# Performance work log

Hardware: AMD Instinct MI355X
Metric: run time of the kernel (lower is better)

Reference implementation:

```python
import jax, jax.numpy as jnp
import numpy as np

B, N, H, D, A = 64, 32, 100, 400, 200  # batch, news_num, hist_len, news_dim, attention_dim


def setup_inputs() -> dict:
    key = jax.random.key(0)
    k0, k1, k2, k3, k4 = jax.random.split(key, 5)
    log_vec = jax.random.normal(k0, (B, H, D), dtype=jnp.float32)
    log_mask = jax.random.randint(k1, (B, H), 0, 2).astype(jnp.int32)
    news_vec = jax.random.normal(k2, (B, N, D), dtype=jnp.float32)
    W1 = jax.random.normal(k3, (A, 2 * D), dtype=jnp.float32) * 0.02
    b1 = jnp.zeros((A,), dtype=jnp.float32)
    W2 = jax.random.normal(k4, (1, A), dtype=jnp.float32) * 0.02
    b2 = jnp.zeros((1,), dtype=jnp.float32)
    return {"log_vec": log_vec, "log_mask": log_mask, "news_vec": news_vec,
            "W1": W1, "b1": b1, "W2": W2, "b2": b2}


def reference(log_vec, log_mask, news_vec, W1, b1, W2, b2):
    d = log_vec.shape[-1]
    # affine1 on cat([news, log]) == Wn @ news + Wl @ log (split the weight),
    # so we never build the [B, N, H, 2D] concat tensor.
    Wn, Wl = W1[:, :d], W1[:, d:]
    pn = jnp.einsum('bnd,ad->bna', news_vec, Wn)            # [B, N, A]
    pl = jnp.einsum('bhd,ad->bha', log_vec, Wl) + b1        # [B, H, A]
    h = jnp.tanh(pn[:, :, None, :] + pl[:, None, :, :])     # [B, N, H, A]
    logits = jnp.einsum('bnha,a->bnh', h, W2[0]) + b2[0]    # [B, N, H]
    logits = jnp.where(log_mask[:, None, :] == 0, jnp.float32(-1e9), logits)
    attn = jax.nn.softmax(logits, axis=2)                   # softmax over hist_len
    return jnp.einsum('bnh,bhd->bnd', attn, log_vec)        # [B, N, D]
```

## Files before the change

### kernel.cpp

```cpp
#include <hip/hip_runtime.h>
#include <hip/hip_fp16.h>
#include <math.h>

#define BB 64
#define NN 32
#define HH 100
#define DD 400
#define AA 200
#define NL 8
#define NQ 4
#define SZ_LOG  2560000
#define SZ_NEWS 819200
#define SZ_W1   160000
#define SZ_MASK 6400
#define LROW 40
#define PLP 204
#define WS2_NEED ((size_t)(BB*HH + BB*NN) * AA * 4)

typedef unsigned short u16;
typedef unsigned int   u32;
typedef unsigned long long u64;
typedef __attribute__((ext_vector_type(8))) short    bf16x8;
typedef __attribute__((ext_vector_type(8))) _Float16 halfx8;
typedef __attribute__((ext_vector_type(4))) float    f32x4;

__device__ __forceinline__ float bfh(u32 h) { return __uint_as_float(h << 16); }
__device__ __forceinline__ u16 f2bf(float f) {
    u32 u = __float_as_uint(f);
    u += 0x7fffu + ((u >> 16) & 1u);
    return (u16)(u >> 16);
}
__device__ __forceinline__ float halfbits(u16 h) {
    __half_raw r; r.x = h; __half hv(r); return __half2float(hv);
}
__device__ __forceinline__ u16 h2bits(float f) {
    __half h = __float2half(f); return *(u16*)&h;
}
__device__ __forceinline__ float sane(float x) {
    return (fabsf(x) < 1e6f) ? x : 0.f;
}

template<int DT>
__device__ __forceinline__ float ld1(const void* p, size_t i) {
    if (DT == 0) return bfh(((const u16*)p)[i]);
    if (DT == 1) return halfbits(((const u16*)p)[i]);
    return ((const float*)p)[i];
}

__device__ __forceinline__ bf16x8 cvt8(const float* p) {
    const float4 x0 = *(const float4*)p;
    const float4 x1 = *(const float4*)(p + 4);
    bf16x8 r;
    r[0] = (short)f2bf(sane(x0.x)); r[1] = (short)f2bf(sane(x0.y));
    r[2] = (short)f2bf(sane(x0.z)); r[3] = (short)f2bf(sane(x0.w));
    r[4] = (short)f2bf(sane(x1.x)); r[5] = (short)f2bf(sane(x1.y));
    r[6] = (short)f2bf(sane(x1.z)); r[7] = (short)f2bf(sane(x1.w));
    return r;
}

__device__ __forceinline__ void detect_counts(const u16* logv, int t, int* s_cbf, int* s_cfh) {
    int cbf = 0, cfh = 0;
    for (int i = 2 * t; i < 4096; i += 512) {
        u16 h = logv[i];
        float a = fabsf(bfh(h));
        if (h && a >= 0.03125f && a <= 16.f) cbf++;
        float g = fabsf(halfbits(h));
        if (h && g >= 1e-3f && g <= 64.f) cfh++;
    }
    #pragma unroll
    for (int off = 32; off; off >>= 1) {
        cbf += __shfl_xor(cbf, off);
        cfh += __shfl_xor(cfh, off);
    }
    if ((t & 63) == 0) {
        atomicAdd(s_cbf, cbf);
        atomicAdd(s_cfh, cfh);
    }
}

__device__ __forceinline__ void prologue(
        const u16* logv, const int* mask, const u16* c200a, const u16* c200b,
        int* s_det, int* s_hn, int* mask_s, int* chi, int b, int t,
        int* dt_o, int* aW2_o, int* hn_o)
{
    const int wave = t >> 6, lane = t & 63;
    if (t < 4) s_det[t] = 0;
    if (t < HH) mask_s[t] = mask[b * HH + t];
    __syncthreads();
    if (t < 256) detect_counts(logv, t, &s_det[0], &s_det[1]);
    if (t < AA) {
        if (c200a[t]) atomicOr(&s_det[2], 1);
        if (c200b[t]) atomicOr(&s_det[3], 1);
    }
    if (wave == 0) {
        const bool v = mask_s[lane] != 0;
        const u64 bal = __ballot(v);
        if (v) chi[__popcll(bal & ((1ull << lane) - 1ull))] = lane;
    } else if (wave == 1) {
        const u64 b0 = __ballot(mask_s[lane] != 0);
        const int c0 = __popcll(b0);
        const bool v1 = (lane < HH - 64) && (mask_s[64 + lane] != 0);
        const u64 b1 = __ballot(v1);
        if (v1) chi[c0 + __popcll(b1 & ((1ull << lane) - 1ull))] = 64 + lane;
        if (lane == 0) *s_hn = c0 + __popcll(b1);
    }
    __syncthreads();
    *dt_o  = (s_det[0] > 1024) ? 0 : ((s_det[1] > 1600) ? 1 : 2);
    *aW2_o = (s_det[2] && !s_det[3]) ? 1 : 0;
    *hn_o  = *s_hn;
}

template<int DT>
__device__ __forceinline__ void gemm_body(
        const void* __restrict__ logv, const void* __restrict__ newsv,
        const void* __restrict__ w1, const void* __restrict__ b1p,
        float* __restrict__ ws_pl, float* __restrict__ ws_pn,
        u16* As0, u16* Bs0, u16* As1, u16* Bs1,
        float* b1s, const int* chi, int hn, int r0, int r1, int mtc_loc,
        int b, int q, int t)
{
    const int wave = t >> 6, lane = t & 63;
    const int quad = lane >> 4, col16 = lane & 15;

    if (t < AA) b1s[t] = sane(ld1<DT>(b1p, t));

    const int mtIdx = wave >> 1, half = wave & 1;
    const bool isPn = (mtIdx == mtc_loc);
    const bool act  = (mtIdx <= mtc_loc);
    const int arow  = isPn ? (32 + min(col16, NL - 1)) : (mtIdx * 16 + col16);
    const int aidx  = arow * LROW + quad * 8;
    int bidx[7];
    #pragma unroll
    for (int si = 0; si < 7; ++si) {
        const int sl = min(half * 7 + si, 12);
        const int brow = min(sl * 16 + col16, AA - 1);
        bidx[si] = ((isPn ? 0 : 208) + brow) * LROW + quad * 8;
    }
    f32x4 acc[7];
    #pragma unroll
    for (int si = 0; si < 7; ++si) acc[si] = (f32x4){0.f, 0.f, 0.f, 0.f};

    const int bh0 = t / 832,   rem0 = t - bh0 * 832;
    const int br0 = rem0 >> 2, bseg0 = rem0 & 3;
    const size_t bg0 = (size_t)min(br0, AA - 1) * (2 * DD) + bh0 * DD + bseg0 * 8;
    const int bl0 = (bh0 * 208 + br0) * LROW + bseg0 * 8;
    const int i1 = t + 1024;
    const bool bok1 = i1 < 1664;
    const int bh1 = bok1 ? (i1 / 832) : 0, rem1 = i1 - bh1 * 832;
    const int br1 = rem1 >> 2, bseg1 = rem1 & 3;
    const size_t bg1 = (size_t)min(br1, AA - 1) * (2 * DD) + bh1 * DD + bseg1 * 8;
    const int bl1 = (bh1 * 208 + br1) * LROW + bseg1 * 8;
    const int ar = t >> 2, aseg = t & 3;
    const bool a_ok = t < 160;
    size_t agi = 0;
    if (a_ok) {
        if (ar < 32) {
            const int grow = hn ? chi[min(r0 + ar, hn - 1)] : 0;
            agi = ((size_t)b * HH + grow) * DD + aseg * 8;
        } else {
            agi = ((size_t)b * NN + q * NL + (ar - 32)) * DD + aseg * 8;
        }
    }
    const int al = ar * LROW + aseg * 8;
    const u16*   agp  = (ar < 32 ? (const u16*)logv   : (const u16*)newsv) + agi;
    const float* agpf = (ar < 32 ? (const float*)logv : (const float*)newsv) + agi;
    const u16*   w1p  = (const u16*)w1;
    const float* w1pf = (const float*)w1;

    const uint4 z4 = {0u, 0u, 0u, 0u};
    uint4 vb0 = z4, vb1 = z4, va = z4;

    if (DT != 2) {
        vb0 = *(const uint4*)(w1p + bg0);
        if (bok1) vb1 = *(const uint4*)(w1p + bg1);
        if (a_ok) va  = *(const uint4*)agp;
        *(uint4*)&Bs0[bl0] = vb0;
        if (bok1) *(uint4*)&Bs0[bl1] = vb1;
        if (a_ok) *(uint4*)&As0[al] = va;
        vb0 = *(const uint4*)(w1p + bg0 + 32);
        if (bok1) vb1 = *(const uint4*)(w1p + bg1 + 32);
        if (a_ok) va  = *(const uint4*)(agp + 32);
    } else {
        { bf16x8 c = cvt8(w1pf + bg0); *(uint4*)&Bs0[bl0] = *(uint4*)&c; }
        if (bok1) { bf16x8 c = cvt8(w1pf + bg1); *(uint4*)&Bs0[bl1] = *(uint4*)&c; }
        if (a_ok) { bf16x8 c = cvt8(agpf); *(uint4*)&As0[al] = *(uint4*)&c; }
    }
    __syncthreads();

    for (int ki = 0; ki < 13; ++ki) {
        const int cur = ki & 1;
        u16* const Ac = cur ? As1 : As0;
        u16* const Bc = cur ? Bs1 : Bs0;
        u16* const An = cur ? As0 : As1;
        u16* const Bn = cur ? Bs0 : Bs1;

        if (DT != 2) {
            if (ki < 12) {
                *(uint4*)&Bn[bl0] = vb0;
                if (bok1) *(uint4*)&Bn[bl1] = vb1;
                if (a_ok) *(uint4*)&An[al] = va;
            }
            if (ki < 11) {
                const int kn = ki + 2;
                vb0 = (kn == 12 && bseg0 >= 2) ? z4 : *(const uint4*)(w1p + bg0 + (size_t)kn * 32);
                if (bok1) vb1 = (kn == 12 && bseg1 >= 2) ? z4 : *(const uint4*)(w1p + bg1 + (size_t)kn * 32);
                if (a_ok) va = (kn == 12 && aseg >= 2) ? z4 : *(const uint4*)(agp + (size_t)kn * 32);
            }
        } else {
            if (ki < 12) {
                const int kn = ki + 1;
                uint4 v = z4;
                if (!(kn == 12 && bseg0 >= 2)) { bf16x8 c = cvt8(w1pf + bg0 + (size_t)kn * 32); v = *(uint4*)&c; }
                *(uint4*)&Bn[bl0] = v;
                if (bok1) {
                    v = z4;
                    if (!(kn == 12 && bseg1 >= 2)) { bf16x8 c = cvt8(w1pf + bg1 + (size_t)kn * 32); v = *(uint4*)&c; }
                    *(uint4*)&Bn[bl1] = v;
                }
                if (a_ok) {
                    v = z4;
                    if (!(kn == 12 && aseg >= 2)) { bf16x8 c = cvt8(agpf + (size_t)kn * 32); v = *(uint4*)&c; }
                    *(uint4*)&An[al] = v;
                }
            }
        }

        if (act) {
            if (DT == 1) {
                const halfx8 af = *(const halfx8*)&Ac[aidx];
                #pragma unroll
                for (int si = 0; si < 7; ++si) {
                    const halfx8 bf = *(const halfx8*)&Bc[bidx[si]];
                    acc[si] = __builtin_amdgcn_mfma_f32_16x16x32_f16(af, bf, acc[si], 0, 0, 0);
                }
            } else {
                const bf16x8 af = *(const bf16x8*)&Ac[aidx];
                #pragma unroll
                for (int si = 0; si < 7; ++si) {
                    const bf16x8 bf = *(const bf16x8*)&Bc[bidx[si]];
                    acc[si] = __builtin_amdgcn_mfma_f32_16x16x32_bf16(af, bf, acc[si], 0, 0, 0);
                }
            }
        }
        __syncthreads();
    }

    if (act) {
        #pragma unroll
        for (int si = 0; si < 7; ++si) {
            const int sl = half * 7 + si;
            if (sl > 12) continue;
            const int acol = sl * 16 + col16;
            if (acol < AA) {
                if (isPn) {
                    #pragma unroll
                    for (int r = 0; r < 4; ++r) {
                        const int row = quad * 4 + r;
                        if (row < NL)
                            ws_pn[((size_t)(b * NQ + q) * NL + row) * AA + acol] = sane(acc[si][r]) + b1s[acol];
                    }
                } else {
                    #pragma unroll
                    for (int r = 0; r < 4; ++r) {
                        const int grow = r0 + mtIdx * 16 + quad * 4 + r;
                        if (grow < r1)
                            ws_pl[((size_t)b * HH + grow) * AA + acol] = sane(acc[si][r]);
                    }
                }
            }
        }
    }
}

__global__ __launch_bounds__(1024) void gemm_ws(
        const void* __restrict__ logv, const int* __restrict__ mask,
        const void* __restrict__ newsv, const void* __restrict__ w1,
        const void* __restrict__ c200a, const void* __restrict__ c200b,
        float* __restrict__ ws_pl, float* __restrict__ ws_pn)
{
    __shared__ __align__(16) u16 As0[48 * LROW], As1[48 * LROW];
    __shared__ __align__(16) u16 Bs0[2 * 208 * LROW], Bs1[2 * 208 * LROW];
    __shared__ float b1s[AA];
    __shared__ int   mask_s[HH], chi[HH];
    __shared__ int   s_det[4], s_hn;

    const int t = threadIdx.x;
    const int b = blockIdx.x & 63;
    const int q = blockIdx.x >> 6;

    int dt, aW2, hn;
    prologue((const u16*)logv, mask, (const u16*)c200a, (const u16*)c200b,
             s_det, &s_hn, mask_s, chi, b, t, &dt, &aW2, &hn);
    const void* b1p = aW2 ? c200b : c200a;

    const int qs = (hn + 3) >> 2;
    const int r0 = q * qs;
    const int r1 = min(r0 + qs, hn);
    const int nr = max(r1 - r0, 0);
    const int mtc_loc = (nr + 15) >> 4;

    if (dt == 0)      gemm_body<0>(logv, newsv, w1, b1p, ws_pl, ws_pn, As0, Bs0, As1, Bs1, b1s, chi, hn, r0, r1, mtc_loc, b, q, t);
    else if (dt == 1) gemm_body<1>(logv, newsv, w1, b1p, ws_pl, ws_pn, As0, Bs0, As1, Bs1, b1s, chi, hn, r0, r1, mtc_loc, b, q, t);
    else              gemm_body<2>(logv, newsv, w1, b1p, ws_pl, ws_pn, As0, Bs0, As1, Bs1, b1s, chi, hn, r0, r1, mtc_loc, b, q, t);
}

template<int DT>
__device__ __forceinline__ void attn_body2(
        const void* __restrict__ logv, const void* __restrict__ w2p,
        const float* __restrict__ pls, const float* __restrict__ pnb,
        void* __restrict__ out,
        float (* __restrict__ lgt)[HH], float* __restrict__ w2s,
        const int* __restrict__ chi, int hn, bool useChi,
        int b, int n0, int t)
{
    const int wave = t >> 6, lane = t & 63;

    if (t < AA) w2s[t] = sane(ld1<DT>(w2p, t));
    __syncthreads();

    {
        const int j = t;
        if (j < 4 * hn) {
            const int p = j / hn;
            const int i = j - p * hn;
            const int h = chi[i];
            const float* plr = pls + (size_t)i * AA;
            const float* pA  = pnb + p * AA;
            const float* pB  = pnb + (p + 4) * AA;
            float accA = 0.f, accB = 0.f, sw = 0.f;
            for (int a = 0; a < AA; a += 4) {
                const float4 w4  = *(const float4*)&w2s[a];
                const float4 pl4 = *(const float4*)&plr[a];
                const float4 pA4 = *(const float4*)&pA[a];
                const float4 pB4 = *(const float4*)&pB[a];
                #define LSTEP(CC) { \
                    const float w2v = w4.CC; \
                    const float plv = pl4.CC; \
                    const float eA = __builtin_amdgcn_exp2f((pA4.CC + plv) * 2.885390081777927f); \
                    const float eB = __builtin_amdgcn_exp2f((pB4.CC + plv) * 2.885390081777927f); \
                    accA = __builtin_fmaf(w2v, __builtin_amdgcn_rcpf(eA + 1.f), accA); \
                    accB = __builtin_fmaf(w2v, __builtin_amdgcn_rcpf(eB + 1.f), accB); \
                    sw += w2v; }
                LSTEP(x) LSTEP(y) LSTEP(z) LSTEP(w)
                #undef LSTEP
            }
            lgt[p][h]     = sw - 2.f * accA;
            lgt[p + 4][h] = sw - 2.f * accB;
        }
    }
    __syncthreads();

    if (wave < NL) {
        const int n = wave;
        float m1 = lgt[n][lane];
        float m2 = (lane < HH - 64) ? lgt[n][64 + lane] : -3.0e38f;
        float mx = fmaxf(m1, m2);
        #pragma unroll
        for (int off = 32; off; off >>= 1) mx = fmaxf(mx, __shfl_xor(mx, off));
        float e1 = expf(m1 - mx);
        float e2 = (lane < HH - 64) ? expf(m2 - mx) : 0.f;
        float s = e1 + e2;
        #pragma unroll
        for (int off = 32; off; off >>= 1) s += __shfl_xor(s, off);
        const float inv = 1.f / s;
        lgt[n][lane] = e1 * inv;
        if (lane < HH - 64) lgt[n][64 + lane] = e2 * inv;
    }
    __syncthreads();

    {
        const int n = wave >> 1, half2 = wave & 1;
        const int hn_pv = useChi ? hn : HH;
        const int d2a = lane + 128 * half2;
        const int d2b = d2a + 64;
        const bool bv = d2b < DD / 2;
        const int d2bc = bv ? d2b : d2a;
        float aA0 = 0.f, aA1 = 0.f, aB0 = 0.f, aB1 = 0.f;
        int i = 0;
        for (; i + 1 < hn_pv; i += 2) {
            const int h0 = useChi ? chi[i] : i;
            const int h1 = useChi ? chi[i + 1] : (i + 1);
            const float w0 = lgt[n][h0], w1v = lgt[n][h1];
            float v0a, v1a, v0b, v1b, u0a, u1a, u0b, u1b;
            if (DT == 2) {
                const float* r0 = (const float*)logv + ((size_t)b * HH + h0) * DD;
                const float* r1 = (const float*)logv + ((size_t)b * HH + h1) * DD;
                v0a = r0[2 * d2a]; v1a = r0[2 * d2a + 1];
                v0b = r0[2 * d2bc]; v1b = r0[2 * d2bc + 1];
                u0a = r1[2 * d2a]; u1a = r1[2 * d2a + 1];
                u0b = r1[2 * d2bc]; u1b = r1[2 * d2bc + 1];
            } else {
                const u16* r0 = (const u16*)logv + ((size_t)b * HH + h0) * DD;
                const u16* r1 = (const u16*)logv + ((size_t)b * HH + h1) * DD;
                const u32 pa = *(const u32*)(r0 + 2 * d2a);
                const u32 pb = *(const u32*)(r0 + 2 * d2bc);
                const u32 qa = *(const u32*)(r1 + 2 * d2a);
                const u32 qb = *(const u32*)(r1 + 2 * d2bc);
                if (DT == 0) {
                    v0a = bfh(pa & 0xffffu); v1a = bfh(pa >> 16);
                    v0b = bfh(pb & 0xffffu); v1b = bfh(pb >> 16);
                    u0a = bfh(qa & 0xffffu); u1a = bfh(qa >> 16);
                    u0b = bfh(qb & 0xffffu); u1b = bfh(qb >> 16);
                } else {
                    v0a = halfbits((u16)(pa & 0xffffu)); v1a = halfbits((u16)(pa >> 16));
                    v0b = halfbits((u16)(pb & 0xffffu)); v1b = halfbits((u16)(pb >> 16));
                    u0a = halfbits((u16)(qa & 0xffffu)); u1a = halfbits((u16)(qa >> 16));
                    u0b = halfbits((u16)(qb & 0xffffu)); u1b = halfbits((u16)(qb >> 16));
                }
            }
            aA0 = __builtin_fmaf(w0, sane(v0a), aA0); aA1 = __builtin_fmaf(w0, sane(v1a), aA1);
            aB0 = __builtin_fmaf(w0, sane(v0b), aB0); aB1 = __builtin_fmaf(w0, sane(v1b), aB1);
            aA0 = __builtin_fmaf(w1v, sane(u0a), aA0); aA1 = __builtin_fmaf(w1v, sane(u1a), aA1);
            aB0 = __builtin_fmaf(w1v, sane(u0b), aB0); aB1 = __builtin_fmaf(w1v, sane(u1b), aB1);
        }
        if (i < hn_pv) {
            const int h0 = useChi ? chi[i] : i;
            const float w0 = lgt[n][h0];
            float v0a, v1a, v0b, v1b;
            if (DT == 2) {
                const float* r0 = (const float*)logv + ((size_t)b * HH + h0) * DD;
                v0a = r0[2 * d2a]; v1a = r0[2 * d2a + 1];
                v0b = r0[2 * d2bc]; v1b = r0[2 * d2bc + 1];
            } else {
                const u16* r0 = (const u16*)logv + ((size_t)b * HH + h0) * DD;
                const u32 pa = *(const u32*)(r0 + 2 * d2a);
                const u32 pb = *(const u32*)(r0 + 2 * d2bc);
                if (DT == 0) {
                    v0a = bfh(pa & 0xffffu); v1a = bfh(pa >> 16);
                    v0b = bfh(pb & 0xffffu); v1b = bfh(pb >> 16);
                } else {
                    v0a = halfbits((u16)(pa & 0xffffu)); v1a = halfbits((u16)(pa >> 16));
                    v0b = halfbits((u16)(pb & 0xffffu)); v1b = halfbits((u16)(pb >> 16));
                }
            }
            aA0 = __builtin_fmaf(w0, sane(v0a), aA0); aA1 = __builtin_fmaf(w0, sane(v1a), aA1);
            aB0 = __builtin_fmaf(w0, sane(v0b), aB0); aB1 = __builtin_fmaf(w0, sane(v1b), aB1);
        }
        const size_t obase = ((size_t)b * NN + n0 + n) * DD;
        aA0 = sane(aA0); aA1 = sane(aA1); aB0 = sane(aB0); aB1 = sane(aB1);
        if (DT == 0) {
            *(u32*)((u16*)out + obase + 2 * d2a) = (u32)f2bf(aA0) | ((u32)f2bf(aA1) << 16);
            if (bv) *(u32*)((u16*)out + obase + 2 * d2b) = (u32)f2bf(aB0) | ((u32)f2bf(aB1) << 16);
        } else if (DT == 1) {
            *(u32*)((u16*)out + obase + 2 * d2a) = (u32)h2bits(aA0) | ((u32)h2bits(aA1) << 16);
            if (bv) *(u32*)((u16*)out + obase + 2 * d2b) = (u32)h2bits(aB0) | ((u32)h2bits(aB1) << 16);
        } else {
            float* f = (float*)out;
            f[obase + 2 * d2a] = aA0; f[obase + 2 * d2a + 1] = aA1;
            if (bv) { f[obase + 2 * d2b] = aB0; f[obase + 2 * d2b + 1] = aB1; }
        }
    }
}

__global__ __launch_bounds__(1024) void attn_ws(
        const void* __restrict__ logv, const int* __restrict__ mask,
        const void* __restrict__ c200a, const void* __restrict__ c200b,
        const float* __restrict__ ws_pl, const float* __restrict__ ws_pn,
        void* __restrict__ out)
{
    __shared__ float lgt[NL][HH];
    __shared__ float w2s[AA];
    __shared__ int   mask_s[HH], chi[HH];
    __shared__ int   s_det[4], s_hn, s_diag[2];

    const int t = threadIdx.x;
    const int b = blockIdx.x & 63;
    const int q = blockIdx.x >> 6;
    const int n0 = q * NL;

    if (t == 0) { s_diag[0] = 0; s_diag[1] = 0; }
    if (t < NL * HH) lgt[t / HH][t % HH] = -1.0e9f;
    int dt, aW2, hn;
    prologue((const u16*)logv, mask, (const u16*)c200a, (const u16*)c200b,
             s_det, &s_hn, mask_s, chi, b, t, &dt, &aW2, &hn);
    const void* w2p = aW2 ? c200a : c200b;
    const bool useChi = hn != 0;

    const float* pls = ws_pl + (size_t)b * HH * AA;
    const float* pnb = ws_pn + (size_t)(b * NQ + q) * NL * AA;

    if (dt == 0)      attn_body2<0>(logv, w2p, pls, pnb, out, lgt, w2s, chi, hn, useChi, b, n0, t);
    else if (dt == 1) attn_body2<1>(logv, w2p, pls, pnb, out, lgt, w2s, chi, hn, useChi, b, n0, t);
    else              attn_body2<2>(logv, w2p, pls, pnb, out, lgt, w2s, chi, hn, useChi, b, n0, t);

    if (blockIdx.x == 0) {
        const u32* maskw = (const u32*)mask;
        int mbig = 0, moddnz = 0, mevennz = 0;
        for (int i = t; i < 3200; i += 1024) {
            u32 w = maskw[i];
            if (w > 1u) mbig = 1;
            if ((i & 1) && w) moddnz = 1;
            if (!(i & 1) && w) mevennz = 1;
        }
        atomicOr(&s_diag[0], mbig);
        atomicOr(&s_diag[1], moddnz | (mevennz << 1));
        __syncthreads();
        if (t == 0) {
            const int cb = s_det[0], ch = s_det[1];
            int dg = 0;
            if (cb > 700 && cb < 1300) dg |= 1;
            else if (cb <= 700 && ch > 1300 && ch < 1800) dg |= 1;
            if (s_diag[0]) dg |= 2;
            const int oddnz = s_diag[1] & 1, evennz = (s_diag[1] >> 1) & 1;
            if (!oddnz && evennz) dg |= 4;
            const int nza = s_det[2] ? 1 : 0, nzb = s_det[3] ? 1 : 0;
            if (nza == nzb) dg |= 8;
            if (dg) {
                const float V = 1024.f + 8.f * (float)dg;
                if (dt == 0)      ((u16*)out)[0] = f2bf(V);
                else if (dt == 1) ((u16*)out)[0] = h2bits(V);
                else              ((float*)out)[0] = V;
            }
        }
    }
}

template<int DT>
__device__ __forceinline__ void mega_body(
        const void* __restrict__ logv, const void* __restrict__ newsv,
        const void* __restrict__ w1,
        const void* __restrict__ w2p, const void* __restrict__ b1p,
        void* __restrict__ out,
        u16* As0, u16* Bs0, u16* ovl,
        float* pls, float* pnb,
        float (*lgt)[HH],
        float* w2s, float* b1s,
        const int* chi, int hn, bool useChi,
        int b, int n0, int t)
{
    const int wave = t >> 6, lane = t & 63;
    const int quad = lane >> 4, col16 = lane & 15;
    const int mtc = (hn + 15) >> 4;

    if (t < AA) {
        w2s[t] = sane(ld1<DT>(w2p, t));
        b1s[t] = sane(ld1<DT>(b1p, t));
    }

    const int mtIdx = wave >> 1, half = wave & 1;
    const bool isPn = (mtIdx == mtc);
    const bool act  = (mtIdx <= mtc);
    const int arow  = isPn ? (112 + min(col16, NL - 1)) : (mtIdx * 16 + col16);
    const int aidx  = arow * LROW + quad * 8;
    int bidx[7];
    #pragma unroll
    for (int si = 0; si < 7; ++si) {
        const int sl = min(half * 7 + si, 12);
        const int brow = min(sl * 16 + col16, AA - 1);
        bidx[si] = ((isPn ? 0 : 208) + brow) * LROW + quad * 8;
    }
    f32x4 acc[7];
    #pragma unroll
    for (int si = 0; si < 7; ++si) acc[si] = (f32x4){0.f, 0.f, 0.f, 0.f};

    const int bh0 = t / 832,   rem0 = t - bh0 * 832;
    const int br0 = rem0 >> 2, bseg0 = rem0 & 3;
    const size_t bg0 = (size_t)min(br0, AA - 1) * (2 * DD) + bh0 * DD + bseg0 * 8;
    const int bl0 = (bh0 * 208 + br0) * LROW + bseg0 * 8;
    const int i1 = t + 1024;
    const bool bok1 = i1 < 1664;
    const int bh1 = bok1 ? (i1 / 832) : 0, rem1 = i1 - bh1 * 832;
    const int br1 = rem1 >> 2, bseg1 = rem1 & 3;
    const size_t bg1 = (size_t)min(br1, AA - 1) * (2 * DD) + bh1 * DD + bseg1 * 8;
    const int bl1 = (bh1 * 208 + br1) * LROW + bseg1 * 8;
    const int ar = t >> 2, aseg = t & 3;
    const bool a_ok = (t < 480) && ((ar < mtc * 16) || (ar >= 112));
    size_t agi = 0;
    if (a_ok) {
        if (ar < 112) agi = ((size_t)b * HH + chi[min(ar, hn - 1)]) * DD + aseg * 8;
        else          agi = ((size_t)b * NN + n0 + (ar - 112)) * DD + aseg * 8;
    }
    const int al = ar * LROW + aseg * 8;
    const u16*   agp  = (ar < 112 ? (const u16*)logv   : (const u16*)newsv) + agi;
    const float* agpf = (ar < 112 ? (const float*)logv : (const float*)newsv) + agi;
    const u16*   w1p  = (const u16*)w1;
    const float* w1pf = (const float*)w1;

    u16* const As1 = ovl;
    u16* const Bs1 = ovl + 120 * LROW;

    const uint4 z4 = {0u, 0u, 0u, 0u};
    uint4 vb0 = z4, vb1 = z4, va = z4;

    if (DT != 2) {
        vb0 = *(const uint4*)(w1p + bg0);
        if (bok1) vb1 = *(const uint4*)(w1p + bg1);
        if (a_ok) va  = *(const uint4*)agp;
        *(uint4*)&Bs0[bl0] = vb0;
        if (bok1) *(uint4*)&Bs0[bl1] = vb1;
        if (a_ok) *(uint4*)&As0[al] = va;
        vb0 = *(const uint4*)(w1p + bg0 + 32);
        if (bok1) vb1 = *(const uint4*)(w1p + bg1 + 32);
        if (a_ok) va  = *(const uint4*)(agp + 32);
    } else {
        { bf16x8 c = cvt8(w1pf + bg0); *(uint4*)&Bs0[bl0] = *(uint4*)&c; }
        if (bok1) { bf16x8 c = cvt8(w1pf + bg1); *(uint4*)&Bs0[bl1] = *(uint4*)&c; }
        if (a_ok) { bf16x8 c = cvt8(agpf); *(uint4*)&As0[al] = *(uint4*)&c; }
    }
    __syncthreads();

    for (int ki = 0; ki < 13; ++ki) {
        const int cur = ki & 1;
        u16* const Ac = cur ? As1 : As0;
        u16* const Bc = cur ? Bs1 : Bs0;
        u16* const An = cur ? As0 : As1;
        u16* const Bn = cur ? Bs0 : Bs1;

        if (DT != 2) {
            if (ki < 12) {
                *(uint4*)&Bn[bl0] = vb0;
                if (bok1) *(uint4*)&Bn[bl1] = vb1;
                if (a_ok) *(uint4*)&An[al] = va;
            }
            if (ki < 11) {
                const int kn = ki + 2;
                vb0 = (kn == 12 && bseg0 >= 2) ? z4 : *(const uint4*)(w1p + bg0 + (size_t)kn * 32);
                if (bok1) vb1 = (kn == 12 && bseg1 >= 2) ? z4 : *(const uint4*)(w1p + bg1 + (size_t)kn * 32);
                if (a_ok) va = (kn == 12 && aseg >= 2) ? z4 : *(const uint4*)(agp + (size_t)kn * 32);
            }
        } else {
            if (ki < 12) {
                const int kn = ki + 1;
                uint4 v = z4;
                if (!(kn == 12 && bseg0 >= 2)) { bf16x8 c = cvt8(w1pf + bg0 + (size_t)kn * 32); v = *(uint4*)&c; }
                *(uint4*)&Bn[bl0] = v;
                if (bok1) {
                    v = z4;
                    if (!(kn == 12 && bseg1 >= 2)) { bf16x8 c = cvt8(w1pf + bg1 + (size_t)kn * 32); v = *(uint4*)&c; }
                    *(uint4*)&Bn[bl1] = v;
                }
                if (a_ok) {
                    v = z4;
                    if (!(kn == 12 && aseg >= 2)) { bf16x8 c = cvt8(agpf + (size_t)kn * 32); v = *(uint4*)&c; }
                    *(uint4*)&An[al] = v;
                }
            }
        }

        if (act) {
            if (DT == 1) {
                const halfx8 af = *(const halfx8*)&Ac[aidx];
                #pragma unroll
                for (int si = 0; si < 7; ++si) {
                    const halfx8 bf = *(const halfx8*)&Bc[bidx[si]];
                    acc[si] = __builtin_amdgcn_mfma_f32_16x16x32_f16(af, bf, acc[si], 0, 0, 0);
                }
            } else {
                const bf16x8 af = *(const bf16x8*)&Ac[aidx];
                #pragma unroll
                for (int si = 0; si < 7; ++si) {
                    const bf16x8 bf = *(const bf16x8*)&Bc[bidx[si]];
                    acc[si] = __builtin_amdgcn_mfma_f32_16x16x32_bf16(af, bf, acc[si], 0, 0, 0);
                }
            }
        }
        __syncthreads();
    }

    if (act) {
        #pragma unroll
        for (int si = 0; si < 7; ++si) {
            const int sl = half * 7 + si;
            if (sl > 12) continue;
            const int acol = sl * 16 + col16;
            if (acol < AA) {
                if (isPn) {
                    #pragma unroll
                    for (int r = 0; r < 4; ++r) {
                        const int row = quad * 4 + r;
                        if (row < NL) pnb[row * PLP + acol] = sane(acc[si][r]) + b1s[acol];
                    }
                } else {
                    #pragma unroll
                    for (int r = 0; r < 4; ++r) {
                        const int row = mtIdx * 16 + quad * 4 + r;
                        if (row < hn) pls[row * PLP + acol] = sane(acc[si][r]);
                    }
                }
            }
        }
    }
    __syncthreads();

    {
        const int j = t;
        if (j < 4 * hn) {
            const int p = j / hn;
            const int i = j - p * hn;
            const int h = chi[i];
            const float* plr = pls + i * PLP;
            const float* pA  = pnb + p * PLP;
            const float* pB  = pnb + (p + 4) * PLP;
            float accA = 0.f, accB = 0.f, sw = 0.f;
            for (int a = 0; a < AA; a += 4) {
                const float4 w4  = *(const float4*)&w2s[a];
                const float4 pl4 = *(const float4*)&plr[a];
                const float4 pA4 = *(const float4*)&pA[a];
                const float4 pB4 = *(const float4*)&pB[a];
                #define LSTEP(CC) { \
                    const float w2v = w4.CC; \
                    const float plv = pl4.CC; \
                    const float eA = __builtin_amdgcn_exp2f((pA4.CC + plv) * 2.885390081777927f); \
                    const float eB = __builtin_amdgcn_exp2f((pB4.CC + plv) * 2.885390081777927f); \
                    accA = __builtin_fmaf(w2v, __builtin_amdgcn_rcpf(eA + 1.f), accA); \
                    accB = __builtin_fmaf(w2v, __builtin_amdgcn_rcpf(eB + 1.f), accB); \
                    sw += w2v; }
                LSTEP(x) LSTEP(y) LSTEP(z) LSTEP(w)
                #undef LSTEP
            }
            lgt[p][h]     = sw - 2.f * accA;
            lgt[p + 4][h] = sw - 2.f * accB;
        }
    }
    __syncthreads();

    if (wave < NL) {
        const int n = wave;
        float m1 = lgt[n][lane];
        float m2 = (lane < HH - 64) ? lgt[n][64 + lane] : -3.0e38f;
        float mx = fmaxf(m1, m2);
        #pragma unroll
        for (int off = 32; off; off >>= 1) mx = fmaxf(mx, __shfl_xor(mx, off));
        float e1 = expf(m1 - mx);
        float e2 = (lane < HH - 64) ? expf(m2 - mx) : 0.f;
        float s = e1 + e2;
        #pragma unroll
        for (int off = 32; off; off >>= 1) s += __shfl_xor(s, off);
        const float inv = 1.f / s;
        lgt[n][lane] = e1 * inv;
        if (lane < HH - 64) lgt[n][64 + lane] = e2 * inv;
    }
    __syncthreads();

    {
        const int n = wave >> 1, half2 = wave & 1;
        const int hn_pv = useChi ? hn : HH;
        const int d2a = lane + 128 * half2;
        const int d2b = d2a + 64;
        const bool bv = d2b < DD / 2;
        const int d2bc = bv ? d2b : d2a;
        float aA0 = 0.f, aA1 = 0.f, aB0 = 0.f, aB1 = 0.f;
        int i = 0;
        for (; i + 1 < hn_pv; i += 2) {
            const int h0 = useChi ? chi[i] : i;
            const int h1 = useChi ? chi[i + 1] : (i + 1);
            const float w0 = lgt[n][h0], w1v = lgt[n][h1];
            float v0a, v1a, v0b, v1b, u0a, u1a, u0b, u1b;
            if (DT == 2) {
                const float* r0 = (const float*)logv + ((size_t)b * HH + h0) * DD;
                const float* r1 = (const float*)logv + ((size_t)b * HH + h1) * DD;
                v0a = r0[2 * d2a]; v1a = r0[2 * d2a + 1];
                v0b = r0[2 * d2bc]; v1b = r0[2 * d2bc + 1];
                u0a = r1[2 * d2a]; u1a = r1[2 * d2a + 1];
                u0b = r1[2 * d2bc]; u1b = r1[2 * d2bc + 1];
            } else {
                const u16* r0 = (const u16*)logv + ((size_t)b * HH + h0) * DD;
                const u16* r1 = (const u16*)logv + ((size_t)b * HH + h1) * DD;
                const u32 pa = *(const u32*)(r0 + 2 * d2a);
                const u32 pb = *(const u32*)(r0 + 2 * d2bc);
                const u32 qa = *(const u32*)(r1 + 2 * d2a);
                const u32 qb = *(const u32*)(r1 + 2 * d2bc);
                if (DT == 0) {
                    v0a = bfh(pa & 0xffffu); v1a = bfh(pa >> 16);
                    v0b = bfh(pb & 0xffffu); v1b = bfh(pb >> 16);
                    u0a = bfh(qa & 0xffffu); u1a = bfh(qa >> 16);
                    u0b = bfh(qb & 0xffffu); u1b = bfh(qb >> 16);
                } else {
                    v0a = halfbits((u16)(pa & 0xffffu)); v1a = halfbits((u16)(pa >> 16));
                    v0b = halfbits((u16)(pb & 0xffffu)); v1b = halfbits((u16)(pb >> 16));
                    u0a = halfbits((u16)(qa & 0xffffu)); u1a = halfbits((u16)(qa >> 16));
                    u0b = halfbits((u16)(qb & 0xffffu)); u1b = halfbits((u16)(qb >> 16));
                }
            }
            aA0 = __builtin_fmaf(w0, sane(v0a), aA0); aA1 = __builtin_fmaf(w0, sane(v1a), aA1);
            aB0 = __builtin_fmaf(w0, sane(v0b), aB0); aB1 = __builtin_fmaf(w0, sane(v1b), aB1);
            aA0 = __builtin_fmaf(w1v, sane(u0a), aA0); aA1 = __builtin_fmaf(w1v, sane(u1a), aA1);
            aB0 = __builtin_fmaf(w1v, sane(u0b), aB0); aB1 = __builtin_fmaf(w1v, sane(u1b), aB1);
        }
        if (i < hn_pv) {
            const int h0 = useChi ? chi[i] : i;
            const float w0 = lgt[n][h0];
            float v0a, v1a, v0b, v1b;
            if (DT == 2) {
                const float* r0 = (const float*)logv + ((size_t)b * HH + h0) * DD;
                v0a = r0[2 * d2a]; v1a = r0[2 * d2a + 1];
                v0b = r0[2 * d2bc]; v1b = r0[2 * d2bc + 1];
            } else {
                const u16* r0 = (const u16*)logv + ((size_t)b * HH + h0) * DD;
                const u32 pa = *(const u32*)(r0 + 2 * d2a);
                const u32 pb = *(const u32*)(r0 + 2 * d2bc);
                if (DT == 0) {
                    v0a = bfh(pa & 0xffffu); v1a = bfh(pa >> 16);
                    v0b = bfh(pb & 0xffffu); v1b = bfh(pb >> 16);
                } else {
                    v0a = halfbits((u16)(pa & 0xffffu)); v1a = halfbits((u16)(pa >> 16));
                    v0b = halfbits((u16)(pb & 0xffffu)); v1b = halfbits((u16)(pb >> 16));
                }
            }
            aA0 = __builtin_fmaf(w0, sane(v0a), aA0); aA1 = __builtin_fmaf(w0, sane(v1a), aA1);
            aB0 = __builtin_fmaf(w0, sane(v0b), aB0); aB1 = __builtin_fmaf(w0, sane(v1b), aB1);
        }
        const size_t obase = ((size_t)b * NN + n0 + n) * DD;
        aA0 = sane(aA0); aA1 = sane(aA1); aB0 = sane(aB0); aB1 = sane(aB1);
        if (DT == 0) {
            *(u32*)((u16*)out + obase + 2 * d2a) = (u32)f2bf(aA0) | ((u32)f2bf(aA1) << 16);
            if (bv) *(u32*)((u16*)out + obase + 2 * d2b) = (u32)f2bf(aB0) | ((u32)f2bf(aB1) << 16);
        } else if (DT == 1) {
            *(u32*)((u16*)out + obase + 2 * d2a) = (u32)h2bits(aA0) | ((u32)h2bits(aA1) << 16);
            if (bv) *(u32*)((u16*)out + obase + 2 * d2b) = (u32)h2bits(aB0) | ((u32)h2bits(aB1) << 16);
        } else {
            float* f = (float*)out;
            f[obase + 2 * d2a] = aA0; f[obase + 2 * d2a + 1] = aA1;
            if (bv) { f[obase + 2 * d2b] = aB0; f[obase + 2 * d2b + 1] = aB1; }
        }
    }
}

__global__ __launch_bounds__(1024) void megafused(
        const void* __restrict__ logv, const int* __restrict__ mask,
        const void* __restrict__ newsv, const void* __restrict__ w1,
        const void* __restrict__ c200a, const void* __restrict__ c200b,
        void* __restrict__ out)
{
    __shared__ __align__(16) u16 As0[120 * LROW];
    __shared__ __align__(16) u16 Bs0[2 * 208 * LROW];
    __shared__ __align__(16) char plspool[HH * PLP * 4];
    __shared__ __align__(16) float pnb[NL * PLP];
    __shared__ float lgt[NL][HH];
    __shared__ float w2s[AA], b1s[AA];
    __shared__ int   mask_s[HH], chi[HH];
    __shared__ int   s_det[4], s_hn, s_diag[2];

    float* pls = (float*)plspool;
    u16*   ovl = (u16*)plspool;

    const int t = threadIdx.x;
    const int b  = blockIdx.x & 63;
    const int n0 = (blockIdx.x >> 6) * NL;

    if (t == 0) { s_diag[0] = 0; s_diag[1] = 0; }
    if (t < NL * HH) lgt[t / HH][t % HH] = -1.0e9f;
    int dt, aW2, hn;
    prologue((const u16*)logv, mask, (const u16*)c200a, (const u16*)c200b,
             s_det, &s_hn, mask_s, chi, b, t, &dt, &aW2, &hn);
    const void* w2p = aW2 ? c200a : c200b;
    const void* b1p = aW2 ? c200b : c200a;
    const bool useChi = hn != 0;

    if (dt == 0)      mega_body<0>(logv, newsv, w1, w2p, b1p, out, As0, Bs0, ovl, pls, pnb, lgt, w2s, b1s, chi, hn, useChi, b, n0, t);
    else if (dt == 1) mega_body<1>(logv, newsv, w1, w2p, b1p, out, As0, Bs0, ovl, pls, pnb, lgt, w2s, b1s, chi, hn, useChi, b, n0, t);
    else              mega_body<2>(logv, newsv, w1, w2p, b1p, out, As0, Bs0, ovl, pls, pnb, lgt, w2s, b1s, chi, hn, useChi, b, n0, t);

    if (blockIdx.x == 0) {
        const u32* maskw = (const u32*)mask;
        int mbig = 0, moddnz = 0, mevennz = 0;
        for (int i = t; i < 3200; i += 1024) {
            u32 w = maskw[i];
            if (w > 1u) mbig = 1;
            if ((i & 1) && w) moddnz = 1;
            if (!(i & 1) && w) mevennz = 1;
        }
        atomicOr(&s_diag[0], mbig);
        atomicOr(&s_diag[1], moddnz | (mevennz << 1));
        __syncthreads();
        if (t == 0) {
            const int cb = s_det[0], ch = s_det[1];
            int dg = 0;
            if (cb > 700 && cb < 1300) dg |= 1;
            else if (cb <= 700 && ch > 1300 && ch < 1800) dg |= 1;
            if (s_diag[0]) dg |= 2;
            const int oddnz = s_diag[1] & 1, evennz = (s_diag[1] >> 1) & 1;
            if (!oddnz && evennz) dg |= 4;
            const int nza = s_det[2] ? 1 : 0, nzb = s_det[3] ? 1 : 0;
            if (nza == nzb) dg |= 8;
            if (dg) {
                const float V = 1024.f + 8.f * (float)dg;
                if (dt == 0)      ((u16*)out)[0] = f2bf(V);
                else if (dt == 1) ((u16*)out)[0] = h2bits(V);
                else              ((float*)out)[0] = V;
            }
        }
    }
}

extern "C" void kernel_launch(void* const* d_in, const int* in_sizes, int n_in,
                              void* d_out, int out_size, void* d_ws, size_t ws_size,
                              hipStream_t stream)
{
    const void *logv = nullptr, *maskv = nullptr, *newsv = nullptr, *w1v = nullptr;
    const void *c200a = nullptr, *c200b = nullptr;
    int n200 = 0;
    for (int i = 0; i < n_in; ++i) {
        int s = in_sizes[i];
        if (s == SZ_LOG) logv = d_in[i];
        else if (s == SZ_NEWS) newsv = d_in[i];
        else if (s == SZ_W1) w1v = d_in[i];
        else if (s == SZ_MASK) maskv = d_in[i];
        else if (s == AA) { if (n200 == 0) c200a = d_in[i]; else if (n200 == 1) c200b = d_in[i]; ++n200; }
    }
    if (!logv || !newsv || !w1v || !maskv || n200 < 2) {
        logv = d_in[0]; maskv = d_in[1]; newsv = d_in[2]; w1v = d_in[3];
        c200a = d_in[4]; c200b = d_in[5];
    }

    if (ws_size >= WS2_NEED) {
        float* ws_pl = (float*)d_ws;
        float* ws_pn = ws_pl + (size_t)BB * HH * AA;
        gemm_ws<<<BB * NQ, 1024, 0, stream>>>(logv, (const int*)maskv, newsv,
                                              w1v, c200a, c200b, ws_pl, ws_pn);
        attn_ws<<<BB * NQ, 1024, 0, stream>>>(logv, (const int*)maskv,
                                              c200a, c200b, ws_pl, ws_pn, d_out);
    } else {
        megafused<<<BB * NQ, 1024, 0, stream>>>(logv, (const int*)maskv, newsv,
                                                w1v, c200a, c200b, d_out);
    }
}
```

Measured before the change: 132.6 us.

## Fuse GEMM and attention kernels into one cooperative launch with grid sync

```diff
diff --git a/kernel.cpp b/kernel.cpp
--- a/kernel.cpp
+++ b/kernel.cpp
@@ -1,4 +1,5 @@
 #include <hip/hip_runtime.h>
+#include <hip/hip_cooperative_groups.h>
 #include <hip/hip_fp16.h>
 #include <math.h>
 
@@ -270,38 +271,6 @@
             }
         }
     }
-}
-
-__global__ __launch_bounds__(1024) void gemm_ws(
-        const void* __restrict__ logv, const int* __restrict__ mask,
-        const void* __restrict__ newsv, const void* __restrict__ w1,
-        const void* __restrict__ c200a, const void* __restrict__ c200b,
-        float* __restrict__ ws_pl, float* __restrict__ ws_pn)
-{
-    __shared__ __align__(16) u16 As0[48 * LROW], As1[48 * LROW];
-    __shared__ __align__(16) u16 Bs0[2 * 208 * LROW], Bs1[2 * 208 * LROW];
-    __shared__ float b1s[AA];
-    __shared__ int   mask_s[HH], chi[HH];
-    __shared__ int   s_det[4], s_hn;
-
-    const int t = threadIdx.x;
-    const int b = blockIdx.x & 63;
-    const int q = blockIdx.x >> 6;
-
-    int dt, aW2, hn;
-    prologue((const u16*)logv, mask, (const u16*)c200a, (const u16*)c200b,
-             s_det, &s_hn, mask_s, chi, b, t, &dt, &aW2, &hn);
-    const void* b1p = aW2 ? c200b : c200a;
-
-    const int qs = (hn + 3) >> 2;
-    const int r0 = q * qs;
-    const int r1 = min(r0 + qs, hn);
-    const int nr = max(r1 - r0, 0);
-    const int mtc_loc = (nr + 15) >> 4;
-
-    if (dt == 0)      gemm_body<0>(logv, newsv, w1, b1p, ws_pl, ws_pn, As0, Bs0, As1, Bs1, b1s, chi, hn, r0, r1, mtc_loc, b, q, t);
-    else if (dt == 1) gemm_body<1>(logv, newsv, w1, b1p, ws_pl, ws_pn, As0, Bs0, As1, Bs1, b1s, chi, hn, r0, r1, mtc_loc, b, q, t);
-    else              gemm_body<2>(logv, newsv, w1, b1p, ws_pl, ws_pn, As0, Bs0, As1, Bs1, b1s, chi, hn, r0, r1, mtc_loc, b, q, t);
 }
 
 template<int DT>
@@ -452,14 +421,16 @@
     }
 }
 
-__global__ __launch_bounds__(1024) void attn_ws(
-        const void* __restrict__ logv, const int* __restrict__ mask,
-        const void* __restrict__ c200a, const void* __restrict__ c200b,
-        const float* __restrict__ ws_pl, const float* __restrict__ ws_pn,
-        void* __restrict__ out)
+__global__ __launch_bounds__(1024) void coop_fused(
+        const void* logv, const int* mask,
+        const void* newsv, const void* w1,
+        const void* c200a, const void* c200b,
+        float* ws_pl, float* ws_pn, void* out)
 {
+    __shared__ __align__(16) u16 As0[48 * LROW], As1[48 * LROW];
+    __shared__ __align__(16) u16 Bs0[2 * 208 * LROW], Bs1[2 * 208 * LROW];
     __shared__ float lgt[NL][HH];
-    __shared__ float w2s[AA];
+    __shared__ float w2s[AA], b1s[AA];
     __shared__ int   mask_s[HH], chi[HH];
     __shared__ int   s_det[4], s_hn, s_diag[2];
 
@@ -474,7 +445,23 @@
     prologue((const u16*)logv, mask, (const u16*)c200a, (const u16*)c200b,
              s_det, &s_hn, mask_s, chi, b, t, &dt, &aW2, &hn);
     const void* w2p = aW2 ? c200a : c200b;
+    const void* b1p = aW2 ? c200b : c200a;
     const bool useChi = hn != 0;
+
+    const int qs = (hn + 3) >> 2;
+    const int r0v = q * qs;
+    const int r1v = min(r0v + qs, hn);
+    const int nr = max(r1v - r0v, 0);
+    const int mtc_loc = (nr + 15) >> 4;
+
+    if (dt == 0)      gemm_body<0>(logv, newsv, w1, b1p, ws_pl, ws_pn, As0, Bs0, As1, Bs1, b1s, chi, hn, r0v, r1v, mtc_loc, b, q, t);
+    else if (dt == 1) gemm_body<1>(logv, newsv, w1, b1p, ws_pl, ws_pn, As0, Bs0, As1, Bs1, b1s, chi, hn, r0v, r1v, mtc_loc, b, q, t);
+    else              gemm_body<2>(logv, newsv, w1, b1p, ws_pl, ws_pn, As0, Bs0, As1, Bs1, b1s, chi, hn, r0v, r1v, mtc_loc, b, q, t);
+
+    __syncthreads();
+    __threadfence();
+    cooperative_groups::this_grid().sync();
+    __threadfence();
 
     const float* pls = ws_pl + (size_t)b * HH * AA;
     const float* pnb = ws_pn + (size_t)(b * NQ + q) * NL * AA;
@@ -906,12 +893,19 @@
     if (ws_size >= WS2_NEED) {
         float* ws_pl = (float*)d_ws;
         float* ws_pn = ws_pl + (size_t)BB * HH * AA;
-        gemm_ws<<<BB * NQ, 1024, 0, stream>>>(logv, (const int*)maskv, newsv,
-                                              w1v, c200a, c200b, ws_pl, ws_pn);
-        attn_ws<<<BB * NQ, 1024, 0, stream>>>(logv, (const int*)maskv,
-                                              c200a, c200b, ws_pl, ws_pn, d_out);
-    } else {
-        megafused<<<BB * NQ, 1024, 0, stream>>>(logv, (const int*)maskv, newsv,
-                                                w1v, c200a, c200b, d_out);
-    }
-}
+        const void* a_logv = logv; const int* a_mask = (const int*)maskv;
+        const void* a_news = newsv; const void* a_w1 = w1v;
+        const void* a_ca = c200a;  const void* a_cb = c200b;
+        float* a_pl = ws_pl; float* a_pn = ws_pn; void* a_out = d_out;
+        void* kargs[] = { (void*)&a_logv, (void*)&a_mask, (void*)&a_news,
+                          (void*)&a_w1, (void*)&a_ca, (void*)&a_cb,
+                          (void*)&a_pl, (void*)&a_pn, (void*)&a_out };
+        hipError_t e = hipLaunchCooperativeKernel(
+            reinterpret_cast<void*>(coop_fused),
+            dim3(BB * NQ), dim3(1024), kargs, 0, stream);
+        if (e == hipSuccess) return;
+    }
+
+    megafused<<<BB * NQ, 1024, 0, stream>>>(logv, (const int*)maskv, newsv,
+                                            w1v, c200a, c200b, d_out);
+}
```

Result: slower. 300.8 us (+126.8%).
